# Kernel tuning notes

Measured on AMD Instinct MI355X. Metric: run time of the kernel, lower is better.

The kernel has to match this reference:

```python
import jax, jax.numpy as jnp
import numpy as np

B, S, D, H = 4, 2048, 1024, 16
HD = D // H

def setup_inputs() -> dict:
    key = jax.random.key(0)
    ks = jax.random.split(key, 5)
    x = jax.random.normal(ks[0], (B, S, D), dtype=jnp.float32)
    # learned params (torch Linear: y = x @ W.T + b)
    s1 = 1.0 / np.sqrt(D)
    Wqkv = jax.random.uniform(ks[1], (3 * D, D), jnp.float32, -s1, s1)
    bqkv = jax.random.uniform(ks[2], (3 * D,), jnp.float32, -s1, s1)
    Wproj = jax.random.uniform(ks[3], (D, D), jnp.float32, -s1, s1)
    bproj = jax.random.uniform(ks[4], (D,), jnp.float32, -s1, s1)
    # causal mask, broadcast over batch and heads; 0 -> masked
    mask = jnp.tril(jnp.ones((S, S), jnp.int32))[None, None]
    return {"x": x, "Wqkv": Wqkv, "bqkv": bqkv, "Wproj": Wproj, "bproj": bproj, "mask": mask}

def reference(x, Wqkv, bqkv, Wproj, bproj, mask):
    b, s, d = x.shape
    qkv = x @ Wqkv.T + bqkv                      # [B,S,3D]
    qkv = qkv.reshape(b, s, 3, H, HD).transpose(2, 0, 3, 1, 4)  # [3,B,H,S,HD]
    q, k, v = qkv[0], qkv[1], qkv[2]
    scores = jnp.einsum('bhqd,bhkd->bhqk', q, k) / np.sqrt(HD).astype(np.float32)
    scores = jnp.where(mask == 0, -jnp.inf, scores)
    attn = jax.nn.softmax(scores, axis=-1)
    ctx = jnp.einsum('bhqk,bhkd->bhqd', attn, v)  # [B,H,S,HD]
    ctx = ctx.transpose(0, 2, 1, 3).reshape(b, s, d)
    return ctx @ Wproj.T + bproj
```

## Files before the change

kernel.cpp:

```cpp
#include <hip/hip_runtime.h>
#include <stdint.h>

typedef __bf16 bf16;
typedef __bf16 bf16x4 __attribute__((ext_vector_type(4)));
typedef __bf16 bf16x8 __attribute__((ext_vector_type(8)));
typedef float f32x4 __attribute__((ext_vector_type(4)));
typedef short short4v __attribute__((ext_vector_type(4)));

#define NB 4
#define NS 2048
#define ND 1024
#define NH 16
#define NHD 64
#define QSCALE 0.1803368801111204f
#define FMAX   8.0f
#define CPITCH 136

typedef const __attribute__((address_space(1))) unsigned GU;
typedef __attribute__((address_space(3))) unsigned LU;

__device__ __forceinline__ bf16x8 load8f(const float* p) {
    float4 a = *(const float4*)p;
    float4 b = *(const float4*)(p + 4);
    bf16x8 r;
    r[0] = (bf16)a.x; r[1] = (bf16)a.y; r[2] = (bf16)a.z; r[3] = (bf16)a.w;
    r[4] = (bf16)b.x; r[5] = (bf16)b.y; r[6] = (bf16)b.z; r[7] = (bf16)b.w;
    return r;
}
__device__ __forceinline__ void store8(bf16* p, bf16x8 v) { *(bf16x8*)p = v; }
__device__ __forceinline__ void store8(float* p, bf16x8 v) {
    float4 a; a.x = (float)v[0]; a.y = (float)v[1]; a.z = (float)v[2]; a.w = (float)v[3];
    float4 b; b.x = (float)v[4]; b.y = (float)v[5]; b.z = (float)v[6]; b.w = (float)v[7];
    *(float4*)p = a; *(float4*)(p + 4) = b;
}

__device__ __forceinline__ f32x4 mfma16(bf16x4 a, bf16x4 b, f32x4 c) {
#ifdef __HIP_DEVICE_COMPILE__
#if __has_builtin(__builtin_amdgcn_mfma_f32_16x16x16bf16_1k)
    return __builtin_amdgcn_mfma_f32_16x16x16bf16_1k(
        __builtin_bit_cast(short4v, a), __builtin_bit_cast(short4v, b), c, 0, 0, 0);
#else
    f32x4 d;
    asm("v_mfma_f32_16x16x16_bf16 %0, %1, %2, %3"
        : "=v"(d) : "v"(a), "v"(b), "v"(c));
    return d;
#endif
#else
    return c;
#endif
}

__device__ __forceinline__ int sw(int row, int col) {
    return row * 72 + (col ^ (((row >> 2) & 3) * 16));
}

__global__ __launch_bounds__(256)
void convert_kernel(const float* __restrict__ s0, bf16* __restrict__ d0, int n0,
                    const float* __restrict__ s1, bf16* __restrict__ d1, int n1,
                    const float* __restrict__ s2, bf16* __restrict__ d2, int n2)
{
    int idx = (blockIdx.x * 256 + threadIdx.x) * 8;
    const float* s; bf16* d;
    if (idx < n0)              { s = s0 + idx;  d = d0 + idx; }
    else if ((idx -= n0) < n1) { s = s1 + idx;  d = d1 + idx; }
    else if ((idx -= n1) < n2) { s = s2 + idx;  d = d2 + idx; }
    else return;
    *(bf16x8*)d = load8f(s);
}

template<typename TO, int MODE>
__device__ __forceinline__ void gemm_epilogue(
    f32x4 (&acc)[4][4], bf16* Ls, const float* __restrict__ bias,
    TO* __restrict__ O0, bf16* __restrict__ O1, bf16* __restrict__ O2,
    int N, int m0, int n0, int tid)
{
    const int lane = tid & 63;
    const int w = tid >> 6, wm = w >> 1, wn = w & 1;
    const int lr = lane & 15, quad = lane >> 4;
    const int cls = (MODE == 0) ? (n0 >> 10) : 1;

    if (MODE == 0 && cls == 2) {
#pragma unroll
        for (int im = 0; im < 4; ++im) {
            int rowb = wm * 64 + im * 16 + quad * 4;
#pragma unroll
            for (int in = 0; in < 4; ++in) {
                int col = wn * 64 + in * 16 + lr;
                float bv = bias[n0 + col];
                bf16x4 pv;
#pragma unroll
                for (int r = 0; r < 4; ++r) pv[r] = (bf16)(acc[im][in][r] + bv);
                *(bf16x4*)&Ls[col * CPITCH + rowb] = pv;
            }
        }
        __syncthreads();
        const int b = m0 >> 11, s0 = m0 & 2047;
#pragma unroll
        for (int p = 0; p < 8; ++p) {
            int idx = tid + 256 * p;
            int col = idx & 127, mg = idx >> 7;
            bf16x8 v8 = *(const bf16x8*)&Ls[col * CPITCH + mg * 8];
            int ncol = n0 + col;
            int h = (ncol >> 6) & 15, hd = ncol & 63;
            *(bf16x8*)&((bf16*)O0)[((size_t)(b * NH + h) * NHD + hd) * NS + s0 + mg * 8] = v8;
        }
    } else {
#pragma unroll
        for (int im = 0; im < 4; ++im) {
            int rowb = wm * 64 + im * 16 + quad * 4;
#pragma unroll
            for (int in = 0; in < 4; ++in) {
                int col = wn * 64 + in * 16 + lr;
                float bv = bias[n0 + col];
#pragma unroll
                for (int r = 0; r < 4; ++r) {
                    float v = acc[im][in][r] + bv;
                    if (MODE == 0 && cls == 0) v *= QSCALE;
                    Ls[(rowb + r) * CPITCH + col] = (bf16)v;
                }
            }
        }
        __syncthreads();
#pragma unroll
        for (int p = 0; p < 8; ++p) {
            int idx = tid + 256 * p;
            int row = idx >> 4, colg = (idx & 15) * 8;
            bf16x8 v8 = *(const bf16x8*)&Ls[row * CPITCH + colg];
            if (MODE == 0) {
                int ncol = n0 + colg;
                int h = (ncol >> 6) & 15, hd = ncol & 63;
                int m = m0 + row, b = m >> 11, s = m & 2047;
                bf16* dst = (cls == 0) ? O1 : O2;
                *(bf16x8*)&dst[((size_t)(b * NH + h) * NS + s) * NHD + hd] = v8;
            } else {
                store8(&O0[(size_t)(m0 + row) * N + n0 + colg], v8);
            }
        }
    }
}

template<typename TO, int MODE>
__global__ __launch_bounds__(256, 3)
void gemm_bt(const bf16* __restrict__ Xp, const bf16* __restrict__ Wp,
             const float* __restrict__ bias, TO* __restrict__ O0,
             bf16* __restrict__ O1, bf16* __restrict__ O2, int N, int K)
{
    __shared__ union {
        struct { bf16 Ah[128 * 32]; bf16 Bh[128 * 32]; } s;
        bf16 C[128 * CPITCH];
    } u;
    const int tid  = threadIdx.x;
    const int lane = tid & 63;
    const int w    = tid >> 6;
    const int wm   = w >> 1, wn = w & 1;
    const int lr   = lane & 15, quad = lane >> 4;
    const int m0   = blockIdx.y * 128;
    const int n0   = blockIdx.x * 128;

    const int srow = w * 32 + (lane >> 2);
    const int scol = (lane & 3) * 8;
    const bf16* gA = Xp + (size_t)(m0 + srow) * K + scol;
    const bf16* gB = Wp + (size_t)(n0 + srow) * K + scol;

    f32x4 acc[4][4] = {};

    for (int k0 = 0; k0 < K; k0 += 32) {
#pragma unroll
        for (int c = 0; c < 2; ++c) {
            __builtin_amdgcn_global_load_lds((GU*)(gA + (size_t)c * 16 * K + k0),
                                             (LU*)&u.s.Ah[(w * 32 + c * 16) * 32], 16, 0, 0);
            __builtin_amdgcn_global_load_lds((GU*)(gB + (size_t)c * 16 * K + k0),
                                             (LU*)&u.s.Bh[(w * 32 + c * 16) * 32], 16, 0, 0);
        }
        __syncthreads();

        bf16x8 af[4], bfr[4];
#pragma unroll
        for (int im = 0; im < 4; ++im)
            af[im] = *(const bf16x8*)(&u.s.Ah[(wm * 64 + im * 16 + lr) * 32 + quad * 8]);
#pragma unroll
        for (int in = 0; in < 4; ++in)
            bfr[in] = *(const bf16x8*)(&u.s.Bh[(wn * 64 + in * 16 + lr) * 32 + quad * 8]);
#pragma unroll
        for (int im = 0; im < 4; ++im)
#pragma unroll
            for (int in = 0; in < 4; ++in)
                acc[im][in] = __builtin_amdgcn_mfma_f32_16x16x32_bf16(
                    af[im], bfr[in], acc[im][in], 0, 0, 0);
        __syncthreads();
    }

    gemm_epilogue<TO, MODE>(acc, u.C, bias, O0, O1, O2, N, m0, n0, tid);
}

__global__ __launch_bounds__(256, 3)
void attn_kernel(const bf16* __restrict__ Q, const bf16* __restrict__ K,
                 const bf16* __restrict__ Vt_g, bf16* __restrict__ ctx)
{
    const int jt = 15 - (blockIdx.x >> 6);
    const int bh = blockIdx.x & 63;
    const int b  = bh >> 4, h = bh & 15;
    const int q0 = jt * 128;
    const bf16* Qp = Q + (size_t)bh * NS * NHD;
    const bf16* Kp = K + (size_t)bh * NS * NHD;
    const bf16* Vp = Vt_g + (size_t)bh * NHD * NS;

    __shared__ union {
        struct { bf16 Kh[64 * 72]; bf16 Vh[64 * 72]; } s;
        bf16 QO[128 * 72];
    } u;

    const int tid  = threadIdx.x;
    const int lane = tid & 63;
    const int w    = tid >> 6;
    const int lr   = lane & 15, quad = lane >> 4;

    const int srow = tid >> 3;
    const int sch  = (tid & 7) * 8;

    bf16x8 kreg[2], vreg[2];
#pragma unroll
    for (int i = 0; i < 2; ++i) {
        kreg[i] = *(const bf16x8*)(Kp + (size_t)(srow + 32 * i) * NHD + sch);
        vreg[i] = *(const bf16x8*)(Vp + (size_t)(srow + 32 * i) * NS + sch);
    }

#pragma unroll
    for (int i = 0; i < 4; ++i) {
        int row = srow + 32 * i;
        *(bf16x8*)(&u.QO[sw(row, sch)]) =
            *(const bf16x8*)(Qp + (size_t)(q0 + row) * NHD + sch);
    }
    __syncthreads();

    bf16x8 qf[2][2];
#pragma unroll
    for (int qg = 0; qg < 2; ++qg)
#pragma unroll
        for (int ks = 0; ks < 2; ++ks)
            qf[qg][ks] = *(const bf16x8*)(&u.QO[sw(w * 32 + qg * 16 + lr, ks * 32 + quad * 8)]);
    __syncthreads();

    float l_part[2] = {0.f, 0.f};
    f32x4 acco[2][4] = {};

    const int wq0 = q0 + w * 32;
    const int nkt = 2 * jt + 2;
    for (int kt = 0; kt < nkt; ++kt) {
#pragma unroll
        for (int i = 0; i < 2; ++i) {
            *(bf16x8*)(&u.s.Kh[sw(srow + 32 * i, sch)]) = kreg[i];
            *(bf16x8*)(&u.s.Vh[sw(srow + 32 * i, sch)]) = vreg[i];
        }
        if (kt + 1 < nkt) {
#pragma unroll
            for (int i = 0; i < 2; ++i) {
                kreg[i] = *(const bf16x8*)(Kp + (size_t)((kt + 1) * 64 + srow + 32 * i) * NHD + sch);
                vreg[i] = *(const bf16x8*)(Vp + (size_t)(srow + 32 * i) * NS + (kt + 1) * 64 + sch);
            }
        }
        __syncthreads();

        if (kt * 64 <= wq0 + 31) {
            f32x4 sacc[2][4] = {};
#pragma unroll
            for (int ks = 0; ks < 2; ++ks) {
#pragma unroll
                for (int kn = 0; kn < 4; ++kn) {
                    bf16x8 ak = *(const bf16x8*)(&u.s.Kh[sw(kn * 16 + lr, ks * 32 + quad * 8)]);
                    sacc[0][kn] = __builtin_amdgcn_mfma_f32_16x16x32_bf16(ak, qf[0][ks], sacc[0][kn], 0, 0, 0);
                    sacc[1][kn] = __builtin_amdgcn_mfma_f32_16x16x32_bf16(ak, qf[1][ks], sacc[1][kn], 0, 0, 0);
                }
            }

            const bool diag = (kt * 64 + 63 > wq0);
            bf16x4 pf[2][4];
#pragma unroll
            for (int qg = 0; qg < 2; ++qg) {
                const int qrow = wq0 + qg * 16 + lr;
#pragma unroll
                for (int kn = 0; kn < 4; ++kn) {
#pragma unroll
                    for (int r = 0; r < 4; ++r) {
                        float x = sacc[qg][kn][r];
                        if (diag) {
                            int kcol = kt * 64 + kn * 16 + quad * 4 + r;
                            x = (kcol <= qrow) ? x : -INFINITY;
                        }
                        float p = __builtin_amdgcn_exp2f(x - FMAX);
                        l_part[qg] += p;
                        pf[qg][kn][r] = (bf16)p;
                    }
                }
            }

#pragma unroll
            for (int kn = 0; kn < 4; ++kn) {
#pragma unroll
                for (int jn = 0; jn < 4; ++jn) {
                    bf16x4 av = *(const bf16x4*)(&u.s.Vh[sw(jn * 16 + lr, kn * 16 + quad * 4)]);
                    acco[0][jn] = mfma16(av, pf[0][kn], acco[0][jn]);
                    acco[1][jn] = mfma16(av, pf[1][kn], acco[1][jn]);
                }
            }
        }
        __syncthreads();
    }

    float rinv[2];
#pragma unroll
    for (int qg = 0; qg < 2; ++qg) {
        float l = l_part[qg];
        l += __shfl_xor(l, 16);
        l += __shfl_xor(l, 32);
        rinv[qg] = 1.0f / l;
    }

    __syncthreads();
#pragma unroll
    for (int qg = 0; qg < 2; ++qg)
#pragma unroll
        for (int jn = 0; jn < 4; ++jn) {
            bf16x4 pv;
#pragma unroll
            for (int r = 0; r < 4; ++r) pv[r] = (bf16)(acco[qg][jn][r] * rinv[qg]);
            *(bf16x4*)&u.QO[(w * 32 + qg * 16 + lr) * 72 + jn * 16 + quad * 4] = pv;
        }
    __syncthreads();
#pragma unroll
    for (int p = 0; p < 4; ++p) {
        int idx = tid + 256 * p;
        int row = idx >> 3, colg = (idx & 7) * 8;
        bf16x8 v8 = *(const bf16x8*)&u.QO[row * 72 + colg];
        *(bf16x8*)&ctx[((size_t)(b * NS) + q0 + row) * ND + h * NHD + colg] = v8;
    }
}

extern "C" void kernel_launch(void* const* d_in, const int* in_sizes, int n_in,
                              void* d_out, int out_size, void* d_ws, size_t ws_size,
                              hipStream_t stream) {
    const float* x     = (const float*)d_in[0];
    const float* Wqkv  = (const float*)d_in[1];
    const float* bqkv  = (const float*)d_in[2];
    const float* Wproj = (const float*)d_in[3];
    const float* bproj = (const float*)d_in[4];
    float* out = (float*)d_out;

    const size_t per = (size_t)NB * NH * NS * NHD;
    bf16* q_ws = (bf16*)d_ws;
    bf16* k_ws = q_ws + per;
    bf16* v_ws = k_ws + per;
    bf16* x_bf = v_ws + per;
    bf16* c_ws = x_bf;
    bf16* wq_bf = x_bf + per;
    bf16* wp_bf = wq_bf + (size_t)3 * ND * ND;

    const int n0 = NB * NS * ND;
    const int n1 = 3 * ND * ND;
    const int n2 = ND * ND;
    convert_kernel<<<(n0 + n1 + n2) / (256 * 8), 256, 0, stream>>>(
        x, x_bf, n0, Wqkv, wq_bf, n1, Wproj, wp_bf, n2);

    dim3 gq(3 * ND / 128, NB * NS / 128);
    gemm_bt<bf16, 0><<<gq, 256, 0, stream>>>(
        x_bf, wq_bf, bqkv, v_ws, q_ws, k_ws, 3 * ND, ND);

    attn_kernel<<<dim3(NB * NH * 16), 256, 0, stream>>>(q_ws, k_ws, v_ws, c_ws);

    dim3 gp(ND / 128, NB * NS / 128);
    gemm_bt<float, 1><<<gp, 256, 0, stream>>>(
        c_ws, wp_bf, bproj, out, nullptr, nullptr, ND, ND);
}
```

Baseline: 264.4 us.

## Replace GEMM with 128x256 double-buffered 512-thread kernel with swizzled LDS

Both projection GEMMs now use a 128x256 output tile with 8 waves, a K step of 64, and double-buffered LDS filled by direct global-to-LDS loads issued two stages ahead, with explicit vmcnt waits and barriers. The LDS layout uses an XOR swizzle to avoid bank conflicts, and MFMA blocks run under raised wave priority. The goal is to hide global load latency and cut barrier and load overhead per MFMA. In exchange it uses much more LDS (96 KB), which lowers occupancy, and the hand-written waitcnt synchronization is fragile.

```diff
diff --git a/kernel.cpp b/kernel.cpp
--- a/kernel.cpp
+++ b/kernel.cpp
@@ -14,10 +14,13 @@
 #define NHD 64
 #define QSCALE 0.1803368801111204f
 #define FMAX   8.0f
-#define CPITCH 136
 
 typedef const __attribute__((address_space(1))) unsigned GU;
 typedef __attribute__((address_space(3))) unsigned LU;
+
+#define WAIT_VM(n) asm volatile("s_waitcnt vmcnt(" #n ")" ::: "memory")
+#define BAR() do { asm volatile("" ::: "memory"); __builtin_amdgcn_s_barrier(); \
+                   asm volatile("" ::: "memory"); } while (0)
 
 __device__ __forceinline__ bf16x8 load8f(const float* p) {
     float4 a = *(const float4*)p;
@@ -69,13 +72,13 @@
 }
 
 template<typename TO, int MODE>
-__device__ __forceinline__ void gemm_epilogue(
+__device__ __forceinline__ void epi256(
     f32x4 (&acc)[4][4], bf16* Ls, const float* __restrict__ bias,
     TO* __restrict__ O0, bf16* __restrict__ O1, bf16* __restrict__ O2,
     int N, int m0, int n0, int tid)
 {
     const int lane = tid & 63;
-    const int w = tid >> 6, wm = w >> 1, wn = w & 1;
+    const int w = tid >> 6, wm = w >> 2, wn = w & 3;
     const int lr = lane & 15, quad = lane >> 4;
     const int cls = (MODE == 0) ? (n0 >> 10) : 1;
 
@@ -90,16 +93,16 @@
                 bf16x4 pv;
 #pragma unroll
                 for (int r = 0; r < 4; ++r) pv[r] = (bf16)(acc[im][in][r] + bv);
-                *(bf16x4*)&Ls[col * CPITCH + rowb] = pv;
+                *(bf16x4*)&Ls[col * 136 + rowb] = pv;
             }
         }
         __syncthreads();
         const int b = m0 >> 11, s0 = m0 & 2047;
 #pragma unroll
         for (int p = 0; p < 8; ++p) {
-            int idx = tid + 256 * p;
-            int col = idx & 127, mg = idx >> 7;
-            bf16x8 v8 = *(const bf16x8*)&Ls[col * CPITCH + mg * 8];
+            int idx = tid + 512 * p;
+            int col = idx >> 4, mg = idx & 15;
+            bf16x8 v8 = *(const bf16x8*)&Ls[col * 136 + mg * 8];
             int ncol = n0 + col;
             int h = (ncol >> 6) & 15, hd = ncol & 63;
             *(bf16x8*)&((bf16*)O0)[((size_t)(b * NH + h) * NHD + hd) * NS + s0 + mg * 8] = v8;
@@ -116,16 +119,16 @@
                 for (int r = 0; r < 4; ++r) {
                     float v = acc[im][in][r] + bv;
                     if (MODE == 0 && cls == 0) v *= QSCALE;
-                    Ls[(rowb + r) * CPITCH + col] = (bf16)v;
+                    Ls[(rowb + r) * 264 + col] = (bf16)v;
                 }
             }
         }
         __syncthreads();
 #pragma unroll
         for (int p = 0; p < 8; ++p) {
-            int idx = tid + 256 * p;
-            int row = idx >> 4, colg = (idx & 15) * 8;
-            bf16x8 v8 = *(const bf16x8*)&Ls[row * CPITCH + colg];
+            int idx = tid + 512 * p;
+            int row = idx >> 5, colg = (idx & 31) * 8;
+            bf16x8 v8 = *(const bf16x8*)&Ls[row * 264 + colg];
             if (MODE == 0) {
                 int ncol = n0 + colg;
                 int h = (ncol >> 6) & 15, hd = ncol & 63;
@@ -140,58 +143,82 @@
 }
 
 template<typename TO, int MODE>
-__global__ __launch_bounds__(256, 3)
-void gemm_bt(const bf16* __restrict__ Xp, const bf16* __restrict__ Wp,
+__global__ __launch_bounds__(512, 2)
+void gemm256(const bf16* __restrict__ Xp, const bf16* __restrict__ Wp,
              const float* __restrict__ bias, TO* __restrict__ O0,
              bf16* __restrict__ O1, bf16* __restrict__ O2, int N, int K)
 {
-    __shared__ union {
-        struct { bf16 Ah[128 * 32]; bf16 Bh[128 * 32]; } s;
-        bf16 C[128 * CPITCH];
-    } u;
+    __shared__ __align__(16) bf16 L[49152];
     const int tid  = threadIdx.x;
     const int lane = tid & 63;
     const int w    = tid >> 6;
-    const int wm   = w >> 1, wn = w & 1;
     const int lr   = lane & 15, quad = lane >> 4;
+    const int wm   = w >> 2, wn = w & 3;
     const int m0   = blockIdx.y * 128;
-    const int n0   = blockIdx.x * 128;
-
-    const int srow = w * 32 + (lane >> 2);
-    const int scol = (lane & 3) * 8;
-    const bf16* gA = Xp + (size_t)(m0 + srow) * K + scol;
-    const bf16* gB = Wp + (size_t)(n0 + srow) * K + scol;
+    const int n0   = blockIdx.x * 256;
+
+    const int lanep = lane ^ ((lane & 32) >> 4);
+    const bf16* gsrc[6]; int ldst[6];
+#pragma unroll
+    for (int j = 0; j < 6; ++j) {
+        int g = w * 6 + j;
+        int isA = g < 16;
+        int gb = isA ? g : g - 16;
+        int c = gb * 64 + lanep;
+        int grow = c >> 3, gcol = (c & 7) * 8;
+        gsrc[j] = (isA ? Xp + (size_t)(m0 + grow) * K
+                       : Wp + (size_t)(n0 + grow) * K) + gcol;
+        ldst[j] = (isA ? 0 : 8192) + gb * 512;
+    }
+
+#define STAGE256(t) do { const int kofs_ = (t) * 64;                           \
+    bf16* Lb_ = &L[((t) & 1) * 24576];                                         \
+    _Pragma("unroll")                                                          \
+    for (int j = 0; j < 6; ++j)                                                \
+        __builtin_amdgcn_global_load_lds((GU*)(gsrc[j] + kofs_),               \
+                                         (LU*)&Lb_[ldst[j]], 16, 0, 0); } while (0)
+
+    const int sb16  = ((lr >> 2) & 1) * 16;
+    const int aoff0 = ((wm * 64 + lr) * 64 + quad * 8) ^ sb16;
+    const int boff0 = (8192 + (wn * 64 + lr) * 64 + quad * 8) ^ sb16;
 
     f32x4 acc[4][4] = {};
-
-    for (int k0 = 0; k0 < K; k0 += 32) {
-#pragma unroll
-        for (int c = 0; c < 2; ++c) {
-            __builtin_amdgcn_global_load_lds((GU*)(gA + (size_t)c * 16 * K + k0),
-                                             (LU*)&u.s.Ah[(w * 32 + c * 16) * 32], 16, 0, 0);
-            __builtin_amdgcn_global_load_lds((GU*)(gB + (size_t)c * 16 * K + k0),
-                                             (LU*)&u.s.Bh[(w * 32 + c * 16) * 32], 16, 0, 0);
-        }
-        __syncthreads();
-
-        bf16x8 af[4], bfr[4];
-#pragma unroll
-        for (int im = 0; im < 4; ++im)
-            af[im] = *(const bf16x8*)(&u.s.Ah[(wm * 64 + im * 16 + lr) * 32 + quad * 8]);
-#pragma unroll
-        for (int in = 0; in < 4; ++in)
-            bfr[in] = *(const bf16x8*)(&u.s.Bh[(wn * 64 + in * 16 + lr) * 32 + quad * 8]);
-#pragma unroll
-        for (int im = 0; im < 4; ++im)
-#pragma unroll
-            for (int in = 0; in < 4; ++in)
-                acc[im][in] = __builtin_amdgcn_mfma_f32_16x16x32_bf16(
-                    af[im], bfr[in], acc[im][in], 0, 0, 0);
-        __syncthreads();
-    }
-
-    gemm_epilogue<TO, MODE>(acc, u.C, bias, O0, O1, O2, N, m0, n0, tid);
-}
+    const int NT = K >> 6;
+
+    STAGE256(0);
+    STAGE256(1);
+    WAIT_VM(6);
+    BAR();
+
+    for (int t = 0; t < NT; ++t) {
+        const int db = (t & 1) * 24576;
+        bf16x8 afr[2][4], bfr[2][4];
+#pragma unroll
+        for (int ks = 0; ks < 2; ++ks)
+#pragma unroll
+            for (int i = 0; i < 4; ++i) {
+                afr[ks][i] = *(const bf16x8*)&L[db + aoff0 + i * 1024 + ks * 32];
+                bfr[ks][i] = *(const bf16x8*)&L[db + boff0 + i * 1024 + ks * 32];
+            }
+        __builtin_amdgcn_s_setprio(1);
+#pragma unroll
+        for (int ks = 0; ks < 2; ++ks)
+#pragma unroll
+            for (int im = 0; im < 4; ++im)
+#pragma unroll
+                for (int in = 0; in < 4; ++in)
+                    acc[im][in] = __builtin_amdgcn_mfma_f32_16x16x32_bf16(
+                        afr[ks][im], bfr[ks][in], acc[im][in], 0, 0, 0);
+        __builtin_amdgcn_s_setprio(0);
+        BAR();
+        if (t + 2 < NT) { STAGE256(t + 2); WAIT_VM(6); }
+        else WAIT_VM(0);
+        BAR();
+    }
+
+    epi256<TO, MODE>(acc, L, bias, O0, O1, O2, N, m0, n0, tid);
+}
+#undef STAGE256
 
 __global__ __launch_bounds__(256, 3)
 void attn_kernel(const bf16* __restrict__ Q, const bf16* __restrict__ K,
@@ -361,13 +388,13 @@
     convert_kernel<<<(n0 + n1 + n2) / (256 * 8), 256, 0, stream>>>(
         x, x_bf, n0, Wqkv, wq_bf, n1, Wproj, wp_bf, n2);
 
-    dim3 gq(3 * ND / 128, NB * NS / 128);
-    gemm_bt<bf16, 0><<<gq, 256, 0, stream>>>(
+    dim3 gq(3 * ND / 256, NB * NS / 128);
+    gemm256<bf16, 0><<<gq, 512, 0, stream>>>(
         x_bf, wq_bf, bqkv, v_ws, q_ws, k_ws, 3 * ND, ND);
 
     attn_kernel<<<dim3(NB * NH * 16), 256, 0, stream>>>(q_ws, k_ws, v_ws, c_ws);
 
-    dim3 gp(ND / 128, NB * NS / 128);
-    gemm_bt<float, 1><<<gp, 256, 0, stream>>>(
+    dim3 gp(ND / 256, NB * NS / 128);
+    gemm256<float, 1><<<gp, 512, 0, stream>>>(
         c_ws, wp_bf, bproj, out, nullptr, nullptr, ND, ND);
 }
```

After: 263.3 us. Within noise of the previous version (-0.4%).
